# Performance work log

Hardware: AMD Instinct MI355X
Metric: run time of the kernel (lower is better)

Reference implementation:

```python
import jax, jax.numpy as jnp
import numpy as np

B, T, H = 2, 1024, 4096
HK, HV, DK, DV = 8, 32, 64, 64
VPK = HV // HK            # value heads per key head = 4
KEY_DIM = HK * DK         # 512
VAL_DIM = HV * DV         # 2048
CONV_DIM = 2 * KEY_DIM + VAL_DIM  # 3072
KSZ = 4
EPS = 1e-5
L2_EPS = 1e-6


def _l2norm(x):
    return x * jax.lax.rsqrt(jnp.sum(x * x, axis=-1, keepdims=True) + L2_EPS)


def setup_inputs() -> dict:
    key = jax.random.key(0)
    ks = jax.random.split(key, 8)
    s = 0.02
    return {
        "hidden_states": jax.random.normal(ks[0], (B, T, H), jnp.float32),
        "W_qkvz": jax.random.normal(ks[1], (H, 2 * KEY_DIM + 2 * VAL_DIM), jnp.float32) * s,
        "W_ba": jax.random.normal(ks[2], (H, 2 * HV), jnp.float32) * s,
        "conv_w": jax.random.normal(ks[3], (CONV_DIM, KSZ), jnp.float32) * 0.1,
        "dt_bias": jnp.ones((HV,), jnp.float32),
        "A_log": jnp.log(jax.random.uniform(ks[4], (HV,), jnp.float32, 1.0, 16.0)),
        "norm_w": jnp.ones((DV,), jnp.float32),
        "W_out": jax.random.normal(ks[5], (VAL_DIM, H), jnp.float32) * s,
    }


def _forward(hidden_states, W_qkvz, W_ba, conv_w, dt_bias, A_log, norm_w, W_out):
    # --- projections ---
    qkvz = hidden_states @ W_qkvz                       # [B,T,5120]
    ba = hidden_states @ W_ba                           # [B,T,64]
    # fix_query_key_value_ordering: per key head [q(Dk), k(Dk), v(vpk*Dv), z(vpk*Dv)]
    qkvz = qkvz.reshape(B, T, HK, 2 * DK + 2 * VPK * DV)
    q = qkvz[..., :DK]                                  # [B,T,HK,DK]
    k = qkvz[..., DK:2 * DK]
    v = qkvz[..., 2 * DK:2 * DK + VPK * DV].reshape(B, T, HV, DV)
    z = qkvz[..., 2 * DK + VPK * DV:].reshape(B, T, HV, DV)
    ba = ba.reshape(B, T, HK, 2 * VPK)
    b = ba[..., :VPK].reshape(B, T, HV)
    a = ba[..., VPK:].reshape(B, T, HV)

    # --- causal depthwise conv over concatenated qkv, then silu ---
    mixed = jnp.concatenate(
        [q.reshape(B, T, KEY_DIM), k.reshape(B, T, KEY_DIM), v.reshape(B, T, VAL_DIM)], axis=-1)
    padded = jnp.pad(mixed, ((0, 0), (KSZ - 1, 0), (0, 0)))
    conv = sum(padded[:, j:j + T, :] * conv_w[:, j] for j in range(KSZ))
    conv = jax.nn.silu(conv)
    q = conv[..., :KEY_DIM].reshape(B, T, HK, DK)
    k = conv[..., KEY_DIM:2 * KEY_DIM].reshape(B, T, HK, DK)
    v = conv[..., 2 * KEY_DIM:].reshape(B, T, HV, DV)

    # --- fused GDN gating: g = -exp(A_log)*softplus(a+dt_bias), beta = sigmoid(b) ---
    g = -jnp.exp(A_log) * jax.nn.softplus(a + dt_bias)  # [B,T,HV]
    beta = jax.nn.sigmoid(b)                            # [B,T,HV]

    # --- q/k l2 norm + scale, broadcast key heads to value heads ---
    q = _l2norm(q) * (DK ** -0.5)
    k = _l2norm(k)
    q = jnp.repeat(q, VPK, axis=2)                      # [B,T,HV,DK]
    k = jnp.repeat(k, VPK, axis=2)

    # --- gated delta-rule recurrence over time ---
    def step(S, inp):
        qt, kt, vt, gt, bt = inp                        # qt/kt [B,HV,DK], vt [B,HV,DV]
        S = S * jnp.exp(gt)[..., None, None]            # decay
        pred = jnp.einsum('bhk,bhkv->bhv', kt, S)
        delta = (vt - pred) * bt[..., None]
        S = S + jnp.einsum('bhk,bhv->bhkv', kt, delta)
        o = jnp.einsum('bhk,bhkv->bhv', qt, S)
        return S, o

    xs = (q.transpose(1, 0, 2, 3), k.transpose(1, 0, 2, 3), v.transpose(1, 0, 2, 3),
          g.transpose(1, 0, 2), beta.transpose(1, 0, 2))
    S0 = jnp.zeros((B, HV, DK, DV), q.dtype)
    _, o = jax.lax.scan(step, S0, xs)                   # [T,B,HV,DV]
    o = o.transpose(1, 0, 2, 3)                         # [B,T,HV,DV]

    # --- gated RMSNorm (norm before gate) + out projection ---
    o_n = o * jax.lax.rsqrt(jnp.mean(o * o, axis=-1, keepdims=True) + EPS) * norm_w
    o_n = o_n * jax.nn.silu(z)
    return o_n.reshape(B, T, VAL_DIM) @ W_out           # [B,T,H]


def reference(hidden_states, W_qkvz, W_ba, conv_w, dt_bias, A_log, norm_w, W_out):
    return _forward(hidden_states, W_qkvz, W_ba, conv_w, dt_bias, A_log, norm_w, W_out)
```

## Files before the change

### kernel.cpp

```cpp
#include <hip/hip_runtime.h>
#include <hip/hip_bf16.h>
#include <cstdint>
#include <cstddef>


typedef __attribute__((ext_vector_type(8))) short short8;
typedef __attribute__((ext_vector_type(4))) float f32x4;

__device__ __forceinline__ short f2bf(float f) {
  union { float f; unsigned u; } x; x.f = f;
  unsigned r = x.u + 0x7fffu + ((x.u >> 16) & 1u);
  return (short)(r >> 16);
}

__device__ __forceinline__ void gl_lds16(const short* g, short* l) {
  __builtin_amdgcn_global_load_lds(
      (const __attribute__((address_space(1))) void*)g,
      (__attribute__((address_space(3))) void*)l, 16, 0, 0);
}

__global__ __launch_bounds__(256) void to_bf16_kernel(const float* __restrict__ x,
                                                      short* __restrict__ y) {
  int i = blockIdx.x * 256 + threadIdx.x;
  float4 v = ((const float4*)x)[i];
  ushort4 r;
  r.x = (unsigned short)f2bf(v.x);
  r.y = (unsigned short)f2bf(v.y);
  r.z = (unsigned short)f2bf(v.z);
  r.w = (unsigned short)f2bf(v.w);
  ((ushort4*)y)[i] = r;
}

__global__ __launch_bounds__(256) void transpose_w1(const float* __restrict__ Wq,
                                                    const float* __restrict__ Wba,
                                                    short* __restrict__ Wt) {
  __shared__ float tile[32][33];
  int n0 = blockIdx.x * 32;
  int k0 = blockIdx.y * 32;
  int t = threadIdx.x;
  int r = t >> 5;
  int c = t & 31;
#pragma unroll
  for (int i = 0; i < 4; ++i) {
    int kl = r + i * 8;
    int n = n0 + c;
    float v = 0.f;
    if (n < 5120) v = Wq[(size_t)(k0 + kl) * 5120 + n];
    else if (n < 5184) v = Wba[(size_t)(k0 + kl) * 64 + (n - 5120)];
    tile[kl][c] = v;
  }
  __syncthreads();
#pragma unroll
  for (int i = 0; i < 4; ++i) {
    int nl = r + i * 8;
    int kl = c;
    Wt[(size_t)(n0 + nl) * 4096 + k0 + kl] = f2bf(tile[kl][nl]);
  }
}

__global__ __launch_bounds__(256) void transpose_w2(const float* __restrict__ W,
                                                    short* __restrict__ Wt) {
  __shared__ float tile[32][33];
  int n0 = blockIdx.x * 32;
  int k0 = blockIdx.y * 32;
  int t = threadIdx.x;
  int r = t >> 5;
  int c = t & 31;
#pragma unroll
  for (int i = 0; i < 4; ++i) {
    int kl = r + i * 8;
    tile[kl][c] = W[(size_t)(k0 + kl) * 4096 + n0 + c];
  }
  __syncthreads();
#pragma unroll
  for (int i = 0; i < 4; ++i) {
    int nl = r + i * 8;
    int kl = c;
    Wt[(size_t)(n0 + nl) * 2048 + k0 + kl] = f2bf(tile[kl][nl]);
  }
}

template <bool GUARD_N>
__global__ __launch_bounds__(256) void gemm128p(const short* __restrict__ A,
                                                const short* __restrict__ Bt,
                                                float* __restrict__ C,
                                                int N, int K, int MT) {
  __shared__ __align__(16) short As[3 * 4096];
  __shared__ __align__(16) short Bs[3 * 4096];
  const int tid = threadIdx.x;
  const int w = tid >> 6, lane = tid & 63;
  const int wm = w >> 1, wn = w & 1;

  const int nwg = gridDim.x;
  const int bid = blockIdx.x;
  const int swz = (bid & 7) * (nwg >> 3) + (bid >> 3);
  const int m0 = (swz % MT) * 128;
  const int n0 = (swz / MT) * 128;

  const int p0 = w * 64 + lane;
  const int rp0 = p0 >> 3, q0 = p0 & 7;
  const int mm0 = q0 ^ (rp0 & 7);
  const int srow = rp0 * 2 + (mm0 >> 2);
  const int scol = (mm0 & 3) << 3;
  const short* Ag = A + (size_t)(m0 + srow) * K + scol;
  const short* Bg = Bt + (size_t)(n0 + srow) * K + scol;
  const size_t rstep = (size_t)64 * K;

  const int fr = lane & 15;
  const int s = lane >> 4;
  int aoff[4], boff[4];
#pragma unroll
  for (int i = 0; i < 4; ++i) {
    int row = wm * 64 + i * 16 + fr;
    int rp = row >> 1;
    int q = (((row & 1) << 2) | s) ^ (rp & 7);
    aoff[i] = (rp * 8 + q) * 8;
  }
#pragma unroll
  for (int j = 0; j < 4; ++j) {
    int row = wn * 64 + j * 16 + fr;
    int rp = row >> 1;
    int q = (((row & 1) << 2) | s) ^ (rp & 7);
    boff[j] = (rp * 8 + q) * 8;
  }

  f32x4 acc[4][4];
#pragma unroll
  for (int i = 0; i < 4; ++i)
#pragma unroll
    for (int j = 0; j < 4; ++j) acc[i][j] = (f32x4){0.f, 0.f, 0.f, 0.f};

  const int NKT = K >> 5;

#define STAGE_A(kt, bb)                                                \
  { const short* g = Ag + (size_t)(kt) * 32;                           \
    gl_lds16(g,         &As[(bb) * 4096 + w * 512]);                   \
    gl_lds16(g + rstep, &As[(bb) * 4096 + 2048 + w * 512]); }
#define STAGE_B(kt, bb)                                                \
  { const short* g = Bg + (size_t)(kt) * 32;                           \
    gl_lds16(g,         &Bs[(bb) * 4096 + w * 512]);                   \
    gl_lds16(g + rstep, &Bs[(bb) * 4096 + 2048 + w * 512]); }

  STAGE_A(0, 0); STAGE_B(0, 0);
  STAGE_A(1, 1); STAGE_B(1, 1);
  asm volatile("s_waitcnt vmcnt(4)" ::: "memory");
  __builtin_amdgcn_s_barrier();
  __builtin_amdgcn_sched_barrier(0);

  int bi = 0;
  for (int kt = 0; kt < NKT; ++kt) {
    int bi2 = bi - 1; if (bi2 < 0) bi2 = 2;
    const short* Ab = &As[bi * 4096];
    const short* Bb = &Bs[bi * 4096];
    short8 af[2], bf[4];
#pragma unroll
    for (int i = 0; i < 2; ++i) af[i] = *(const short8*)&Ab[aoff[i]];
#pragma unroll
    for (int j = 0; j < 4; ++j) bf[j] = *(const short8*)&Bb[boff[j]];
    if (kt + 2 < NKT) STAGE_A(kt + 2, bi2);
    __builtin_amdgcn_s_barrier();
    asm volatile("s_waitcnt lgkmcnt(0)" ::: "memory");
    __builtin_amdgcn_sched_barrier(0);
    __builtin_amdgcn_s_setprio(1);
#pragma unroll
    for (int i = 0; i < 2; ++i)
#pragma unroll
      for (int j = 0; j < 4; ++j)
        acc[i][j] = __builtin_amdgcn_mfma_f32_16x16x32_bf16(af[i], bf[j], acc[i][j], 0, 0, 0);
    __builtin_amdgcn_s_setprio(0);
    __builtin_amdgcn_sched_barrier(0);
#pragma unroll
    for (int i = 0; i < 2; ++i) af[i] = *(const short8*)&Ab[aoff[i + 2]];
    if (kt + 2 < NKT) STAGE_B(kt + 2, bi2);
    if (kt < NKT - 2) { asm volatile("s_waitcnt vmcnt(4)" ::: "memory"); }
    else              { asm volatile("s_waitcnt vmcnt(0)" ::: "memory"); }
    __builtin_amdgcn_s_barrier();
    asm volatile("s_waitcnt lgkmcnt(0)" ::: "memory");
    __builtin_amdgcn_sched_barrier(0);
    __builtin_amdgcn_s_setprio(1);
#pragma unroll
    for (int i = 0; i < 2; ++i)
#pragma unroll
      for (int j = 0; j < 4; ++j)
        acc[i + 2][j] = __builtin_amdgcn_mfma_f32_16x16x32_bf16(af[i], bf[j], acc[i + 2][j], 0, 0, 0);
    __builtin_amdgcn_s_setprio(0);
    __builtin_amdgcn_sched_barrier(0);
    __builtin_amdgcn_s_barrier();
    ++bi; if (bi == 3) bi = 0;
  }
#undef STAGE_A
#undef STAGE_B

  const int rbase = (lane >> 4) << 2;
#pragma unroll
  for (int i = 0; i < 4; ++i) {
#pragma unroll
    for (int j = 0; j < 4; ++j) {
      int col = n0 + wn * 64 + j * 16 + fr;
      if (GUARD_N && col >= N) continue;
      int row = m0 + wm * 64 + i * 16 + rbase;
#pragma unroll
      for (int r = 0; r < 4; ++r)
        C[(size_t)(row + r) * N + col] = acc[i][j][r];
    }
  }
}

__global__ __launch_bounds__(256) void conv_kernel(const float* __restrict__ qkvz,
                                                   const float* __restrict__ conv_w,
                                                   float* __restrict__ mix) {
  __shared__ float sq[1024];
  __shared__ float scale[16];
  int bt = blockIdx.x;
  int t = bt & 1023;
  int tid = threadIdx.x;
  for (int c = tid; c < 3072; c += 256) {
    int col;
    if (c < 512) {
      col = (c >> 6) * 640 + (c & 63);
    } else if (c < 1024) {
      int c2 = c - 512;
      col = (c2 >> 6) * 640 + 64 + (c2 & 63);
    } else {
      int c3 = c - 1024;
      int hv = c3 >> 6;
      col = (hv >> 2) * 640 + 128 + (hv & 3) * 64 + (c3 & 63);
    }
    float acc = 0.f;
#pragma unroll
    for (int j = 0; j < 4; ++j) {
      int tt = t - 3 + j;
      if (tt >= 0) acc += qkvz[(size_t)(bt - 3 + j) * 5184 + col] * conv_w[c * 4 + j];
    }
    float sv = acc / (1.f + __expf(-acc));
    if (c < 1024)
      sq[c] = sv;
    else
      mix[(size_t)bt * 3072 + c] = sv;
  }
  __syncthreads();
  int g = tid >> 4, l = tid & 15;
  float p = 0.f;
#pragma unroll
  for (int i = 0; i < 4; ++i) {
    float v = sq[g * 64 + l * 4 + i];
    p += v * v;
  }
  p += __shfl_xor(p, 1);
  p += __shfl_xor(p, 2);
  p += __shfl_xor(p, 4);
  p += __shfl_xor(p, 8);
  if (l == 0) scale[g] = rsqrtf(p + 1e-6f);
  __syncthreads();
  for (int c = tid; c < 1024; c += 256) {
    float s = scale[c >> 6] * ((c < 512) ? 0.125f : 1.f);
    mix[(size_t)bt * 3072 + c] = sq[c] * s;
  }
}

__global__ __launch_bounds__(256) void gate_kernel(const float* __restrict__ qkvz,
                                                   const float* __restrict__ dt_bias,
                                                   const float* __restrict__ A_log,
                                                   float* __restrict__ gb,
                                                   float* __restrict__ beta) {
  int i = blockIdx.x * 256 + threadIdx.x;
  int hv = i & 31;
  int bt = i >> 5;
  int hk = hv >> 2, vp = hv & 3;
  const float* row = qkvz + (size_t)bt * 5184 + 5120 + hk * 8;
  float bv = row[vp];
  float av = row[4 + vp];
  float x = av + dt_bias[hv];
  float sp = (x > 20.f) ? x : log1pf(expf(x));
  gb[i] = -expf(A_log[hv]) * sp;
  beta[i] = 1.f / (1.f + expf(-bv));
}

__global__ __launch_bounds__(256) void precompute_kernel(
    const float* __restrict__ mix, const float* __restrict__ gbuf,
    const float* __restrict__ betab, float* __restrict__ Wbuf,
    float* __restrict__ Pbuf, float* __restrict__ Rbuf, float* __restrict__ cbuf) {
  __shared__ float Kt[64][68];
  __shared__ float Vb[64][68];
  __shared__ float AM[64][68];
  __shared__ float Mm[64][68];
  __shared__ float Tb[16][17];
  __shared__ float cs[64], bb[64];

  const int u = blockIdx.x;
  const int chunk = u & 15, hv = (u >> 4) & 31, b = u >> 9;
  const int hk = hv >> 2;
  const int t0g = b * 1024 + chunk * 64;
  const int tid = threadIdx.x;
  const int tr = tid >> 2, q4 = tid & 3;

  {
    const float* mrow = mix + (size_t)(t0g + tr) * 3072;
#pragma unroll
    for (int e = 0; e < 4; ++e) {
      int c0 = q4 * 16 + e * 4;
      float4 kv = *(const float4*)(mrow + 512 + hk * 64 + c0);
      Kt[c0 + 0][tr] = kv.x; Kt[c0 + 1][tr] = kv.y;
      Kt[c0 + 2][tr] = kv.z; Kt[c0 + 3][tr] = kv.w;
      *(float4*)&Vb[tr][c0] = *(const float4*)(mrow + 1024 + hv * 64 + c0);
    }
  }
  if (tid < 64) {
    cs[tid] = gbuf[(size_t)(t0g + tid) * 32 + hv];
    bb[tid] = betab[(size_t)(t0g + tid) * 32 + hv];
  }
  __syncthreads();
  for (int off = 1; off < 64; off <<= 1) {
    float v = 0.f;
    if (tid < 64 && tid >= off) v = cs[tid - off];
    __syncthreads();
    if (tid < 64) cs[tid] += v;
    __syncthreads();
  }
  if (tid < 64) cbuf[(size_t)u * 64 + tid] = cs[tid];

  {
    float acc[16];
#pragma unroll
    for (int i = 0; i < 16; ++i) acc[i] = 0.f;
    for (int d = 0; d < 64; ++d) {
      float kv = Kt[d][tr];
#pragma unroll
      for (int e = 0; e < 4; ++e) {
        float4 ks = *(const float4*)&Kt[d][q4 * 16 + e * 4];
        acc[e * 4 + 0] += kv * ks.x; acc[e * 4 + 1] += kv * ks.y;
        acc[e * 4 + 2] += kv * ks.z; acc[e * 4 + 3] += kv * ks.w;
      }
    }
    float bt_ = bb[tr], ct_ = cs[tr];
#pragma unroll
    for (int j = 0; j < 16; ++j) {
      int s = q4 * 16 + j;
      AM[tr][s] = (s < tr) ? bt_ * acc[j] * __expf(ct_ - cs[s]) : 0.f;
    }
  }
  __syncthreads();

  for (int i = tid; i < 64 * 68; i += 256) (&Mm[0][0])[i] = 0.f;
  __syncthreads();
  if (tid < 64) {
    int blk = tid >> 4, j = tid & 15, base = blk * 16;
    Mm[base][base + j] = (j == 0) ? 1.f : 0.f;
    for (int r = 1; r < 16; ++r) {
      float sum = 0.f;
      for (int s = 0; s < r; ++s) sum += AM[base + r][base + s] * Mm[base + s][base + j];
      Mm[base + r][base + j] = ((r == j) ? 1.f : 0.f) - sum;
    }
  }
  __syncthreads();
  for (int d = 1; d < 4; ++d) {
    for (int j = 0; j + d < 4; ++j) {
      int i = j + d;
      int r = tid >> 4, c = tid & 15;
      float tsum = 0.f;
      for (int kb = j; kb < i; ++kb)
        for (int uu = 0; uu < 16; ++uu)
          tsum += AM[i * 16 + r][kb * 16 + uu] * Mm[kb * 16 + uu][j * 16 + c];
      Tb[r][c] = tsum;
      __syncthreads();
      float msum = 0.f;
      for (int uu = 0; uu < 16; ++uu)
        msum += Mm[i * 16 + r][i * 16 + uu] * Tb[uu][c];
      __syncthreads();
      Mm[i * 16 + r][j * 16 + c] = -msum;
      __syncthreads();
    }
  }

  {
    const float* mrow = mix + (size_t)(t0g + tr) * 3072 + hk * 64;
#pragma unroll
    for (int e = 0; e < 4; ++e) {
      int c0 = q4 * 16 + e * 4;
      float4 qv = *(const float4*)(mrow + c0);
      AM[c0 + 0][tr] = qv.x; AM[c0 + 1][tr] = qv.y;
      AM[c0 + 2][tr] = qv.z; AM[c0 + 3][tr] = qv.w;
    }
  }
  __syncthreads();

  {
    float acc[16];
#pragma unroll
    for (int i = 0; i < 16; ++i) acc[i] = 0.f;
    for (int d = 0; d < 64; ++d) {
      float qv = AM[d][tr];
#pragma unroll
      for (int e = 0; e < 4; ++e) {
        float4 ks = *(const float4*)&Kt[d][q4 * 16 + e * 4];
        acc[e * 4 + 0] += qv * ks.x; acc[e * 4 + 1] += qv * ks.y;
        acc[e * 4 + 2] += qv * ks.z; acc[e * 4 + 3] += qv * ks.w;
      }
    }
    float ct_ = cs[tr];
#pragma unroll
    for (int e = 0; e < 4; ++e) {
      int s0 = q4 * 16 + e * 4;
      float4 pv;
      pv.x = (s0 + 0 <= tr) ? acc[e * 4 + 0] * __expf(ct_ - cs[s0 + 0]) : 0.f;
      pv.y = (s0 + 1 <= tr) ? acc[e * 4 + 1] * __expf(ct_ - cs[s0 + 1]) : 0.f;
      pv.z = (s0 + 2 <= tr) ? acc[e * 4 + 2] * __expf(ct_ - cs[s0 + 2]) : 0.f;
      pv.w = (s0 + 3 <= tr) ? acc[e * 4 + 3] * __expf(ct_ - cs[s0 + 3]) : 0.f;
      *(float4*)&Pbuf[(size_t)u * 4096 + tr * 64 + s0] = pv;
    }
  }
  __syncthreads();

  {
    float vals[16];
#pragma unroll
    for (int j = 0; j < 16; ++j) vals[j] = Kt[q4 * 16 + j][tr];
    float sc = bb[tr] * __expf(cs[tr]);
    __syncthreads();
#pragma unroll
    for (int j = 0; j < 16; ++j) Kt[tr][q4 * 16 + j] = vals[j] * sc;
  }
  __syncthreads();

  {
    float acc[16];
#pragma unroll
    for (int i = 0; i < 16; ++i) acc[i] = 0.f;
    for (int s = 0; s < 64; ++s) {
      float m = Mm[tr][s];
#pragma unroll
      for (int e = 0; e < 4; ++e) {
        float4 kk = *(const float4*)&Kt[s][q4 * 16 + e * 4];
        acc[e * 4 + 0] += m * kk.x; acc[e * 4 + 1] += m * kk.y;
        acc[e * 4 + 2] += m * kk.z; acc[e * 4 + 3] += m * kk.w;
      }
    }
#pragma unroll
    for (int e = 0; e < 4; ++e) {
      float4 wv = {acc[e * 4 + 0], acc[e * 4 + 1], acc[e * 4 + 2], acc[e * 4 + 3]};
      *(float4*)&Wbuf[(size_t)u * 4096 + tr * 64 + q4 * 16 + e * 4] = wv;
    }
  }
  {
    float acc[16];
#pragma unroll
    for (int i = 0; i < 16; ++i) acc[i] = 0.f;
    for (int s = 0; s < 64; ++s) {
      float m = Mm[tr][s] * bb[s];
#pragma unroll
      for (int e = 0; e < 4; ++e) {
        float4 vv = *(const float4*)&Vb[s][q4 * 16 + e * 4];
        acc[e * 4 + 0] += m * vv.x; acc[e * 4 + 1] += m * vv.y;
        acc[e * 4 + 2] += m * vv.z; acc[e * 4 + 3] += m * vv.w;
      }
    }
#pragma unroll
    for (int e = 0; e < 4; ++e) {
      float4 rv = {acc[e * 4 + 0], acc[e * 4 + 1], acc[e * 4 + 2], acc[e * 4 + 3]};
      *(float4*)&Rbuf[(size_t)u * 4096 + tr * 64 + q4 * 16 + e * 4] = rv;
    }
  }
}

__global__ __launch_bounds__(256) void precompute2_kernel(
    const float* __restrict__ mix, const float* __restrict__ cbuf,
    float* __restrict__ Wbuf, float* __restrict__ Pbuf, float* __restrict__ Rbuf,
    float* __restrict__ Hbuf) {
  __shared__ float At[64][132];
  __shared__ float Bsm[64][188];

  const int u = blockIdx.x;
  const int chunk = u & 15, hv = (u >> 4) & 31, b = u >> 9;
  const int hk = hv >> 2;
  const int t0g = b * 1024 + chunk * 64;
  const int tid = threadIdx.x;
  const int tr = tid >> 2, q4 = tid & 3;

  const float c63 = cbuf[(size_t)u * 64 + 63];
  const float csr = cbuf[(size_t)u * 64 + tr];
  const float sKv = __expf(c63 - csr);

  {
    const float* Pr = Pbuf + (size_t)u * 4096 + tr * 64;
#pragma unroll
    for (int e = 0; e < 4; ++e) {
      int k0 = q4 * 16 + e * 4;
      float4 p4 = *(const float4*)(Pr + k0);
      At[k0 + 0][tr] = p4.x; At[k0 + 1][tr] = p4.y;
      At[k0 + 2][tr] = p4.z; At[k0 + 3][tr] = p4.w;
    }
    const float* Kr = mix + (size_t)(t0g + tr) * 3072 + 512 + hk * 64;
#pragma unroll
    for (int e = 0; e < 4; ++e) {
      int n = q4 * 16 + e * 4;
      float4 k4 = *(const float4*)(Kr + n);
      float4 o4 = {k4.x * sKv, k4.y * sKv, k4.z * sKv, k4.w * sKv};
      *(float4*)&At[tr][64 + n] = o4;
    }
  }
  {
    const float* Wr = Wbuf + (size_t)u * 4096 + tr * 64;
    const float* Rr = Rbuf + (size_t)u * 4096 + tr * 64;
#pragma unroll
    for (int e = 0; e < 4; ++e) {
      int n = q4 * 16 + e * 4;
      int cp = n + ((n >> 3) << 2);
      *(float4*)&Bsm[tr][cp] = *(const float4*)(Wr + n);
      *(float4*)&Bsm[tr][cp + 96] = *(const float4*)(Rr + n);
    }
  }
  __syncthreads();

  const int m0 = (tid >> 4) << 3;
  const int n0 = (tid & 15) << 3;
  const int cb = n0 + ((n0 >> 3) << 2);
  float acc[8][8];
#pragma unroll
  for (int i = 0; i < 8; ++i)
#pragma unroll
    for (int j = 0; j < 8; ++j) acc[i][j] = 0.f;

  for (int k = 0; k < 64; ++k) {
    float4 a0 = *(const float4*)&At[k][m0];
    float4 a1 = *(const float4*)&At[k][m0 + 4];
    float4 b0 = *(const float4*)&Bsm[k][cb];
    float4 b1 = *(const float4*)&Bsm[k][cb + 4];
    float am[8] = {a0.x, a0.y, a0.z, a0.w, a1.x, a1.y, a1.z, a1.w};
    float bn[8] = {b0.x, b0.y, b0.z, b0.w, b1.x, b1.y, b1.z, b1.w};
#pragma unroll
    for (int i = 0; i < 8; ++i)
#pragma unroll
      for (int j = 0; j < 8; ++j) acc[i][j] += am[i] * bn[j];
  }

  if (m0 < 64) {
    if (n0 < 64) {
#pragma unroll
      for (int i = 0; i < 8; ++i) {
        int t = m0 + i;
        float ee = __expf(cbuf[(size_t)u * 64 + t]);
        const float* Qr = mix + (size_t)(t0g + t) * 3072 + hk * 64 + n0;
        float4 q0 = *(const float4*)(Qr);
        float4 q1 = *(const float4*)(Qr + 4);
        float4 g0 = {q0.x * ee - acc[i][0], q0.y * ee - acc[i][1],
                     q0.z * ee - acc[i][2], q0.w * ee - acc[i][3]};
        float4 g1 = {q1.x * ee - acc[i][4], q1.y * ee - acc[i][5],
                     q1.z * ee - acc[i][6], q1.w * ee - acc[i][7]};
        float* dst = Wbuf + (size_t)u * 4096 + t * 64 + n0;
        *(float4*)dst = g0; *(float4*)(dst + 4) = g1;
      }
    } else {
#pragma unroll
      for (int i = 0; i < 8; ++i) {
        float* dst = Rbuf + (size_t)u * 4096 + (m0 + i) * 64 + (n0 - 64);
        float4 r0 = {acc[i][0], acc[i][1], acc[i][2], acc[i][3]};
        float4 r1 = {acc[i][4], acc[i][5], acc[i][6], acc[i][7]};
        *(float4*)dst = r0; *(float4*)(dst + 4) = r1;
      }
    }
  } else {
    if (n0 < 64) {
#pragma unroll
      for (int i = 0; i < 8; ++i) {
        float* dst = Hbuf + (size_t)u * 4096 + (m0 - 64 + i) * 64 + n0;
        float4 h0 = {acc[i][0], acc[i][1], acc[i][2], acc[i][3]};
        float4 h1 = {acc[i][4], acc[i][5], acc[i][6], acc[i][7]};
        *(float4*)dst = h0; *(float4*)(dst + 4) = h1;
      }
    } else {
#pragma unroll
      for (int i = 0; i < 8; ++i) {
        float* dst = Pbuf + (size_t)u * 4096 + (m0 - 64 + i) * 64 + (n0 - 64);
        float4 k0v = {acc[i][0], acc[i][1], acc[i][2], acc[i][3]};
        float4 k1v = {acc[i][4], acc[i][5], acc[i][6], acc[i][7]};
        *(float4*)dst = k0v; *(float4*)(dst + 4) = k1v;
      }
    }
  }
}

__global__ __launch_bounds__(1024) void chunk_scan_kernel(
    const float* __restrict__ Gbuf, const float* __restrict__ Hbuf,
    const float* __restrict__ ORbuf, const float* __restrict__ KRbuf,
    const float* __restrict__ cbuf, float* __restrict__ o) {
  __shared__ float Gs[64][72], Hs[64][72];
  __shared__ float St[16][68];

  const int bid = blockIdx.x;
  const int vs = bid & 3, hv = (bid >> 2) & 31, b = bid >> 7;
  const int bh = b * 32 + hv;
  const int ubase = bh * 16;
  const int tid = threadIdx.x;
  const int tr = tid >> 4, cc = tid & 15;

  (&St[0][0])[tid] = 0.f;
  if (tid < 64) (&St[0][0])[1024 + tid] = 0.f;

  float4 GN, HN;
  float ORn = 0.f, KRn = 0.f, e63n = 0.f;

#define ISSUE(ch)                                                               \
  {                                                                             \
    size_t uu = (size_t)(ubase + (ch));                                         \
    GN = ((const float4*)(Gbuf + uu * 4096))[tid];                              \
    HN = ((const float4*)(Hbuf + uu * 4096))[tid];                              \
    ORn = ORbuf[uu * 4096 + tr * 64 + vs * 16 + cc];                            \
    KRn = KRbuf[uu * 4096 + tr * 64 + vs * 16 + cc];                            \
    e63n = cbuf[uu * 64 + 63];                                                  \
  }

  ISSUE(0);
  *(float4*)&Gs[tr][cc * 4] = GN;
  *(float4*)&Hs[tr][cc * 4] = HN;
  float ORv = ORn, KRv = KRn;
  float e63 = __expf(e63n);
  __syncthreads();

  for (int c = 0; c < 16; ++c) {
    if (c < 15) ISSUE(c + 1);
    float op = ORv, sn = KRv;
    float sold = St[cc][tr];
#pragma unroll
    for (int i = 0; i < 16; ++i) {
      float4 g4 = *(const float4*)&Gs[tr][i * 4];
      float4 h4 = *(const float4*)&Hs[tr][i * 4];
      float4 s4 = *(const float4*)&St[cc][i * 4];
      op += g4.x * s4.x + g4.y * s4.y + g4.z * s4.z + g4.w * s4.w;
      sn -= h4.x * s4.x + h4.y * s4.y + h4.z * s4.z + h4.w * s4.w;
    }
    o[((size_t)(bh * 4 + vs) * 1024 + c * 64 + tr) * 16 + cc] = op;
    float snew = sold * e63 + sn;
    __syncthreads();
    St[cc][tr] = snew;
    if (c < 15) {
      *(float4*)&Gs[tr][cc * 4] = GN;
      *(float4*)&Hs[tr][cc * 4] = HN;
      ORv = ORn; KRv = KRn; e63 = __expf(e63n);
    }
    __syncthreads();
  }
#undef ISSUE
}

__global__ __launch_bounds__(256) void rms_gate_kernel(const float* __restrict__ o,
                                                       const float* __restrict__ qkvz,
                                                       const float* __restrict__ norm_w,
                                                       short* __restrict__ on) {
  int bid = blockIdx.x;
  int bh = bid >> 8;
  int tg = bid & 255;
  int b = bh >> 5, hv = bh & 31;
  int t = tg * 4 + (threadIdx.x >> 6);
  int d = threadIdx.x & 63;
  int bt = b * 1024 + t;
  int hk = hv >> 2, vp = hv & 3;
  float x = o[((size_t)(bh * 4 + (d >> 4)) * 1024 + t) * 16 + (d & 15)];
  float ss = x * x;
  ss += __shfl_xor(ss, 1);
  ss += __shfl_xor(ss, 2);
  ss += __shfl_xor(ss, 4);
  ss += __shfl_xor(ss, 8);
  ss += __shfl_xor(ss, 16);
  ss += __shfl_xor(ss, 32);
  float sc = rsqrtf(ss * (1.f / 64.f) + 1e-5f);
  float z = qkvz[(size_t)bt * 5184 + hk * 640 + 384 + vp * 64 + d];
  float val = x * sc * norm_w[d] * (z / (1.f + __expf(-z)));
  on[((size_t)bt * 32 + hv) * 64 + d] = f2bf(val);
}

extern "C" void kernel_launch(void* const* d_in, const int* in_sizes, int n_in,
                              void* d_out, int out_size, void* d_ws, size_t ws_size,
                              hipStream_t stream) {
  const float* hidden = (const float*)d_in[0];
  const float* W_qkvz = (const float*)d_in[1];
  const float* W_ba = (const float*)d_in[2];
  const float* conv_w = (const float*)d_in[3];
  const float* dt_bias = (const float*)d_in[4];
  const float* A_log = (const float*)d_in[5];
  const float* norm_w = (const float*)d_in[6];
  const float* W_out = (const float*)d_in[7];
  float* out = (float*)d_out;

  char* ws = (char*)d_ws;
  short* A_bf = (short*)(ws + 0);
  float* Hbuf = (float*)(ws + 0);
  short* Wt1 = (short*)(ws + 16777216);
  short* Wt2 = (short*)(ws + 59768832);
  float* qkvz = (float*)(ws + 76546048);
  float* mix = (float*)(ws + 119013376);
  float* gbuf = (float*)(ws + 144179200);
  float* beta = (float*)(ws + 144441344);
  float* o = (float*)(ws + 144703488);
  short* on = (short*)(ws + 161480704);
  float* Wbuf = (float*)(ws + 169869312);
  float* Pbuf = (float*)(ws + 186646528);
  float* Rbuf = (float*)(ws + 203423744);
  float* cbuf = (float*)(ws + 220200960);

  to_bf16_kernel<<<8192, 256, 0, stream>>>(hidden, A_bf);
  transpose_w1<<<dim3(164, 128), 256, 0, stream>>>(W_qkvz, W_ba, Wt1);
  transpose_w2<<<dim3(128, 64), 256, 0, stream>>>(W_out, Wt2);
  gemm128p<true><<<656, 256, 0, stream>>>(A_bf, Wt1, qkvz, 5184, 4096, 16);
  conv_kernel<<<2048, 256, 0, stream>>>(qkvz, conv_w, mix);
  gate_kernel<<<256, 256, 0, stream>>>(qkvz, dt_bias, A_log, gbuf, beta);
  precompute_kernel<<<1024, 256, 0, stream>>>(mix, gbuf, beta, Wbuf, Pbuf, Rbuf, cbuf);
  precompute2_kernel<<<1024, 256, 0, stream>>>(mix, cbuf, Wbuf, Pbuf, Rbuf, Hbuf);
  chunk_scan_kernel<<<256, 1024, 0, stream>>>(Wbuf, Hbuf, Rbuf, Pbuf, cbuf, o);
  rms_gate_kernel<<<16384, 256, 0, stream>>>(o, qkvz, norm_w, on);
  gemm128p<false><<<512, 256, 0, stream>>>(on, Wt2, out, 4096, 2048, 16);
}
```

Baseline: 529.6 us.

## Use 256x128 tile GEMM for the input projection

Adds a new bf16 MFMA GEMM kernel with 256x128 output tiles (each wave computing 128x64) and a triple-buffered LDS pipeline. The A-fragment loads are split into two halves interleaved with the B staging, and the QKVZ projection is switched to it with half as many workgroups. The larger tile is meant to cut global/LDS traffic per FLOP and raise arithmetic intensity. In exchange it uses more registers and LDS per block, and with 328 blocks the GPU may be less evenly occupied.

```diff
diff --git a/kernel.cpp b/kernel.cpp
--- a/kernel.cpp
+++ b/kernel.cpp
@@ -77,6 +77,134 @@
     int nl = r + i * 8;
     int kl = c;
     Wt[(size_t)(n0 + nl) * 2048 + k0 + kl] = f2bf(tile[kl][nl]);
+  }
+}
+
+template <bool GUARD_N>
+__global__ __launch_bounds__(256) void gemm256x128p(const short* __restrict__ A,
+                                                    const short* __restrict__ Bt,
+                                                    float* __restrict__ C,
+                                                    int N, int K, int MT) {
+  __shared__ __align__(16) short As[3 * 8192];
+  __shared__ __align__(16) short Bs[3 * 4096];
+  const int tid = threadIdx.x;
+  const int w = tid >> 6, lane = tid & 63;
+  const int wm = w >> 1, wn = w & 1;
+
+  const int nwg = gridDim.x;
+  const int bid = blockIdx.x;
+  const int swz = (bid & 7) * (nwg >> 3) + (bid >> 3);
+  const int m0 = (swz % MT) * 256;
+  const int n0 = (swz / MT) * 128;
+
+  const int p0 = w * 64 + lane;
+  const int rp0 = p0 >> 3, q0 = p0 & 7;
+  const int mm0 = q0 ^ (rp0 & 7);
+  const int srow = rp0 * 2 + (mm0 >> 2);
+  const int scol = (mm0 & 3) << 3;
+  const short* Ag = A + (size_t)(m0 + srow) * K + scol;
+  const short* Bg = Bt + (size_t)(n0 + srow) * K + scol;
+  const size_t rstep = (size_t)64 * K;
+
+  const int fr = lane & 15;
+  const int s = lane >> 4;
+  int aoff[8], boff[4];
+#pragma unroll
+  for (int i = 0; i < 8; ++i) {
+    int row = wm * 128 + i * 16 + fr;
+    int rp = row >> 1;
+    int q = (((row & 1) << 2) | s) ^ (rp & 7);
+    aoff[i] = (rp * 8 + q) * 8;
+  }
+#pragma unroll
+  for (int j = 0; j < 4; ++j) {
+    int row = wn * 64 + j * 16 + fr;
+    int rp = row >> 1;
+    int q = (((row & 1) << 2) | s) ^ (rp & 7);
+    boff[j] = (rp * 8 + q) * 8;
+  }
+
+  f32x4 acc[8][4];
+#pragma unroll
+  for (int i = 0; i < 8; ++i)
+#pragma unroll
+    for (int j = 0; j < 4; ++j) acc[i][j] = (f32x4){0.f, 0.f, 0.f, 0.f};
+
+  const int NKT = K >> 5;
+
+#define STAGE_A(kt, bb)                                                \
+  { const short* g = Ag + (size_t)(kt) * 32;                           \
+    gl_lds16(g,             &As[(bb) * 8192 + w * 512]);               \
+    gl_lds16(g + rstep,     &As[(bb) * 8192 + 2048 + w * 512]);        \
+    gl_lds16(g + 2 * rstep, &As[(bb) * 8192 + 4096 + w * 512]);        \
+    gl_lds16(g + 3 * rstep, &As[(bb) * 8192 + 6144 + w * 512]); }
+#define STAGE_B(kt, bb)                                                \
+  { const short* g = Bg + (size_t)(kt) * 32;                           \
+    gl_lds16(g,         &Bs[(bb) * 4096 + w * 512]);                   \
+    gl_lds16(g + rstep, &Bs[(bb) * 4096 + 2048 + w * 512]); }
+
+  STAGE_A(0, 0); STAGE_B(0, 0);
+  STAGE_A(1, 1); STAGE_B(1, 1);
+  asm volatile("s_waitcnt vmcnt(6)" ::: "memory");
+  __builtin_amdgcn_s_barrier();
+  __builtin_amdgcn_sched_barrier(0);
+
+  int bi = 0;
+  for (int kt = 0; kt < NKT; ++kt) {
+    int bi2 = bi - 1; if (bi2 < 0) bi2 = 2;
+    const short* Ab = &As[bi * 8192];
+    const short* Bb = &Bs[bi * 4096];
+    short8 af[4], bf[4];
+#pragma unroll
+    for (int i = 0; i < 4; ++i) af[i] = *(const short8*)&Ab[aoff[i]];
+#pragma unroll
+    for (int j = 0; j < 4; ++j) bf[j] = *(const short8*)&Bb[boff[j]];
+    if (kt + 2 < NKT) STAGE_A(kt + 2, bi2);
+    __builtin_amdgcn_s_barrier();
+    asm volatile("s_waitcnt lgkmcnt(0)" ::: "memory");
+    __builtin_amdgcn_sched_barrier(0);
+    __builtin_amdgcn_s_setprio(1);
+#pragma unroll
+    for (int i = 0; i < 4; ++i)
+#pragma unroll
+      for (int j = 0; j < 4; ++j)
+        acc[i][j] = __builtin_amdgcn_mfma_f32_16x16x32_bf16(af[i], bf[j], acc[i][j], 0, 0, 0);
+    __builtin_amdgcn_s_setprio(0);
+    __builtin_amdgcn_sched_barrier(0);
+#pragma unroll
+    for (int i = 0; i < 4; ++i) af[i] = *(const short8*)&Ab[aoff[i + 4]];
+    if (kt + 2 < NKT) STAGE_B(kt + 2, bi2);
+    if (kt < NKT - 2) { asm volatile("s_waitcnt vmcnt(6)" ::: "memory"); }
+    else              { asm volatile("s_waitcnt vmcnt(0)" ::: "memory"); }
+    __builtin_amdgcn_s_barrier();
+    asm volatile("s_waitcnt lgkmcnt(0)" ::: "memory");
+    __builtin_amdgcn_sched_barrier(0);
+    __builtin_amdgcn_s_setprio(1);
+#pragma unroll
+    for (int i = 0; i < 4; ++i)
+#pragma unroll
+      for (int j = 0; j < 4; ++j)
+        acc[i + 4][j] = __builtin_amdgcn_mfma_f32_16x16x32_bf16(af[i], bf[j], acc[i + 4][j], 0, 0, 0);
+    __builtin_amdgcn_s_setprio(0);
+    __builtin_amdgcn_sched_barrier(0);
+    __builtin_amdgcn_s_barrier();
+    ++bi; if (bi == 3) bi = 0;
+  }
+#undef STAGE_A
+#undef STAGE_B
+
+  const int rbase = (lane >> 4) << 2;
+#pragma unroll
+  for (int i = 0; i < 8; ++i) {
+#pragma unroll
+    for (int j = 0; j < 4; ++j) {
+      int col = n0 + wn * 64 + j * 16 + fr;
+      if (GUARD_N && col >= N) continue;
+      int row = m0 + wm * 128 + i * 16 + rbase;
+#pragma unroll
+      for (int r = 0; r < 4; ++r)
+        C[(size_t)(row + r) * N + col] = acc[i][j][r];
+    }
   }
 }
 
@@ -700,7 +828,7 @@
   to_bf16_kernel<<<8192, 256, 0, stream>>>(hidden, A_bf);
   transpose_w1<<<dim3(164, 128), 256, 0, stream>>>(W_qkvz, W_ba, Wt1);
   transpose_w2<<<dim3(128, 64), 256, 0, stream>>>(W_out, Wt2);
-  gemm128p<true><<<656, 256, 0, stream>>>(A_bf, Wt1, qkvz, 5184, 4096, 16);
+  gemm256x128p<true><<<328, 256, 0, stream>>>(A_bf, Wt1, qkvz, 5184, 4096, 8);
   conv_kernel<<<2048, 256, 0, stream>>>(qkvz, conv_w, mix);
   gate_kernel<<<256, 256, 0, stream>>>(qkvz, dt_bias, A_log, gbuf, beta);
   precompute_kernel<<<1024, 256, 0, stream>>>(mix, gbuf, beta, Wbuf, Pbuf, Rbuf, cbuf);
```

Measured after the change: 534.8 us. About the same (+1.0%).

## Use two-wave 128x128 GEMM tiles and halve chunk-scan threads with two columns each

Applied to the files above, without the earlier changes.

The GEMM drops from 4 waves to 2 waves per 128x128 tile. Each wave now computes a 64x128 sub-tile with a 4x8 MFMA accumulator grid, loads 4 A and 8 B fragments per k-step, and issues 4 global-to-LDS loads per stage. The chunk scan kernel goes from 1024 to 512 threads, each computing two state columns, so every G/H fragment read from LDS is reused twice, and the Gs/Hs padding changes. The aim is more work per wave and less LDS traffic per flop, at the cost of higher register pressure (128 accumulator floats per lane) and fewer waves to hide latency.

```diff
diff --git a/kernel.cpp b/kernel.cpp
--- a/kernel.cpp
+++ b/kernel.cpp
@@ -81,15 +81,14 @@
 }
 
 template <bool GUARD_N>
-__global__ __launch_bounds__(256) void gemm128p(const short* __restrict__ A,
-                                                const short* __restrict__ Bt,
-                                                float* __restrict__ C,
-                                                int N, int K, int MT) {
+__global__ __launch_bounds__(128) void gemm128w2(const short* __restrict__ A,
+                                                 const short* __restrict__ Bt,
+                                                 float* __restrict__ C,
+                                                 int N, int K, int MT) {
   __shared__ __align__(16) short As[3 * 4096];
   __shared__ __align__(16) short Bs[3 * 4096];
   const int tid = threadIdx.x;
   const int w = tid >> 6, lane = tid & 63;
-  const int wm = w >> 1, wn = w & 1;
 
   const int nwg = gridDim.x;
   const int bid = blockIdx.x;
@@ -97,53 +96,56 @@
   const int m0 = (swz % MT) * 128;
   const int n0 = (swz / MT) * 128;
 
-  const int p0 = w * 64 + lane;
-  const int rp0 = p0 >> 3, q0 = p0 & 7;
+  const int rp0 = tid >> 3, q0 = tid & 7;
   const int mm0 = q0 ^ (rp0 & 7);
   const int srow = rp0 * 2 + (mm0 >> 2);
   const int scol = (mm0 & 3) << 3;
   const short* Ag = A + (size_t)(m0 + srow) * K + scol;
   const short* Bg = Bt + (size_t)(n0 + srow) * K + scol;
-  const size_t rstep = (size_t)64 * K;
+  const size_t rstep = (size_t)32 * K;
 
   const int fr = lane & 15;
   const int s = lane >> 4;
-  int aoff[4], boff[4];
+  int aoff[4], boff[8];
 #pragma unroll
   for (int i = 0; i < 4; ++i) {
-    int row = wm * 64 + i * 16 + fr;
+    int row = w * 64 + i * 16 + fr;
     int rp = row >> 1;
     int q = (((row & 1) << 2) | s) ^ (rp & 7);
     aoff[i] = (rp * 8 + q) * 8;
   }
 #pragma unroll
-  for (int j = 0; j < 4; ++j) {
-    int row = wn * 64 + j * 16 + fr;
+  for (int j = 0; j < 8; ++j) {
+    int row = j * 16 + fr;
     int rp = row >> 1;
     int q = (((row & 1) << 2) | s) ^ (rp & 7);
     boff[j] = (rp * 8 + q) * 8;
   }
 
-  f32x4 acc[4][4];
+  f32x4 acc[4][8];
 #pragma unroll
   for (int i = 0; i < 4; ++i)
 #pragma unroll
-    for (int j = 0; j < 4; ++j) acc[i][j] = (f32x4){0.f, 0.f, 0.f, 0.f};
+    for (int j = 0; j < 8; ++j) acc[i][j] = (f32x4){0.f, 0.f, 0.f, 0.f};
 
   const int NKT = K >> 5;
 
-#define STAGE_A(kt, bb)                                                \
-  { const short* g = Ag + (size_t)(kt) * 32;                           \
-    gl_lds16(g,         &As[(bb) * 4096 + w * 512]);                   \
-    gl_lds16(g + rstep, &As[(bb) * 4096 + 2048 + w * 512]); }
-#define STAGE_B(kt, bb)                                                \
-  { const short* g = Bg + (size_t)(kt) * 32;                           \
-    gl_lds16(g,         &Bs[(bb) * 4096 + w * 512]);                   \
-    gl_lds16(g + rstep, &Bs[(bb) * 4096 + 2048 + w * 512]); }
+#define STAGE_A(kt, bb)                                                  \
+  { const short* g = Ag + (size_t)(kt) * 32;                             \
+    gl_lds16(g,             &As[(bb) * 4096 + (w << 9)]);                \
+    gl_lds16(g + rstep,     &As[(bb) * 4096 + 1024 + (w << 9)]);         \
+    gl_lds16(g + 2 * rstep, &As[(bb) * 4096 + 2048 + (w << 9)]);         \
+    gl_lds16(g + 3 * rstep, &As[(bb) * 4096 + 3072 + (w << 9)]); }
+#define STAGE_B(kt, bb)                                                  \
+  { const short* g = Bg + (size_t)(kt) * 32;                             \
+    gl_lds16(g,             &Bs[(bb) * 4096 + (w << 9)]);                \
+    gl_lds16(g + rstep,     &Bs[(bb) * 4096 + 1024 + (w << 9)]);         \
+    gl_lds16(g + 2 * rstep, &Bs[(bb) * 4096 + 2048 + (w << 9)]);         \
+    gl_lds16(g + 3 * rstep, &Bs[(bb) * 4096 + 3072 + (w << 9)]); }
 
   STAGE_A(0, 0); STAGE_B(0, 0);
   STAGE_A(1, 1); STAGE_B(1, 1);
-  asm volatile("s_waitcnt vmcnt(4)" ::: "memory");
+  asm volatile("s_waitcnt vmcnt(8)" ::: "memory");
   __builtin_amdgcn_s_barrier();
   __builtin_amdgcn_sched_barrier(0);
 
@@ -152,9 +154,9 @@
     int bi2 = bi - 1; if (bi2 < 0) bi2 = 2;
     const short* Ab = &As[bi * 4096];
     const short* Bb = &Bs[bi * 4096];
-    short8 af[2], bf[4];
-#pragma unroll
-    for (int i = 0; i < 2; ++i) af[i] = *(const short8*)&Ab[aoff[i]];
+    short8 af[4], bf[4];
+#pragma unroll
+    for (int i = 0; i < 4; ++i) af[i] = *(const short8*)&Ab[aoff[i]];
 #pragma unroll
     for (int j = 0; j < 4; ++j) bf[j] = *(const short8*)&Bb[boff[j]];
     if (kt + 2 < NKT) STAGE_A(kt + 2, bi2);
@@ -163,26 +165,26 @@
     __builtin_amdgcn_sched_barrier(0);
     __builtin_amdgcn_s_setprio(1);
 #pragma unroll
-    for (int i = 0; i < 2; ++i)
+    for (int i = 0; i < 4; ++i)
 #pragma unroll
       for (int j = 0; j < 4; ++j)
         acc[i][j] = __builtin_amdgcn_mfma_f32_16x16x32_bf16(af[i], bf[j], acc[i][j], 0, 0, 0);
     __builtin_amdgcn_s_setprio(0);
     __builtin_amdgcn_sched_barrier(0);
 #pragma unroll
-    for (int i = 0; i < 2; ++i) af[i] = *(const short8*)&Ab[aoff[i + 2]];
+    for (int j = 0; j < 4; ++j) bf[j] = *(const short8*)&Bb[boff[j + 4]];
     if (kt + 2 < NKT) STAGE_B(kt + 2, bi2);
-    if (kt < NKT - 2) { asm volatile("s_waitcnt vmcnt(4)" ::: "memory"); }
+    if (kt < NKT - 2) { asm volatile("s_waitcnt vmcnt(8)" ::: "memory"); }
     else              { asm volatile("s_waitcnt vmcnt(0)" ::: "memory"); }
     __builtin_amdgcn_s_barrier();
     asm volatile("s_waitcnt lgkmcnt(0)" ::: "memory");
     __builtin_amdgcn_sched_barrier(0);
     __builtin_amdgcn_s_setprio(1);
 #pragma unroll
-    for (int i = 0; i < 2; ++i)
+    for (int i = 0; i < 4; ++i)
 #pragma unroll
       for (int j = 0; j < 4; ++j)
-        acc[i + 2][j] = __builtin_amdgcn_mfma_f32_16x16x32_bf16(af[i], bf[j], acc[i + 2][j], 0, 0, 0);
+        acc[i][j + 4] = __builtin_amdgcn_mfma_f32_16x16x32_bf16(af[i], bf[j], acc[i][j + 4], 0, 0, 0);
     __builtin_amdgcn_s_setprio(0);
     __builtin_amdgcn_sched_barrier(0);
     __builtin_amdgcn_s_barrier();
@@ -195,10 +197,10 @@
 #pragma unroll
   for (int i = 0; i < 4; ++i) {
 #pragma unroll
-    for (int j = 0; j < 4; ++j) {
-      int col = n0 + wn * 64 + j * 16 + fr;
+    for (int j = 0; j < 8; ++j) {
+      int col = n0 + j * 16 + fr;
       if (GUARD_N && col >= N) continue;
-      int row = m0 + wm * 64 + i * 16 + rbase;
+      int row = m0 + w * 64 + i * 16 + rbase;
 #pragma unroll
       for (int r = 0; r < 4; ++r)
         C[(size_t)(row + r) * N + col] = acc[i][j][r];
@@ -579,11 +581,11 @@
   }
 }
 
-__global__ __launch_bounds__(1024) void chunk_scan_kernel(
+__global__ __launch_bounds__(512) void chunk_scan_kernel(
     const float* __restrict__ Gbuf, const float* __restrict__ Hbuf,
     const float* __restrict__ ORbuf, const float* __restrict__ KRbuf,
     const float* __restrict__ cbuf, float* __restrict__ o) {
-  __shared__ float Gs[64][72], Hs[64][72];
+  __shared__ float Gs[64][68], Hs[64][68];
   __shared__ float St[16][68];
 
   const int bid = blockIdx.x;
@@ -591,55 +593,73 @@
   const int bh = b * 32 + hv;
   const int ubase = bh * 16;
   const int tid = threadIdx.x;
-  const int tr = tid >> 4, cc = tid & 15;
-
-  (&St[0][0])[tid] = 0.f;
-  if (tid < 64) (&St[0][0])[1024 + tid] = 0.f;
-
-  float4 GN, HN;
-  float ORn = 0.f, KRn = 0.f, e63n = 0.f;
+  const int tr = tid >> 3, q8 = tid & 7;
+  const int c0 = q8 * 2, c1 = q8 * 2 + 1;
+
+  for (int i = tid; i < 16 * 68; i += 512) (&St[0][0])[i] = 0.f;
+
+  float4 GN[2], HN[2];
+  float2 ORn, KRn;
+  float e63n = 0.f;
 
 #define ISSUE(ch)                                                               \
   {                                                                             \
     size_t uu = (size_t)(ubase + (ch));                                         \
-    GN = ((const float4*)(Gbuf + uu * 4096))[tid];                              \
-    HN = ((const float4*)(Hbuf + uu * 4096))[tid];                              \
-    ORn = ORbuf[uu * 4096 + tr * 64 + vs * 16 + cc];                            \
-    KRn = KRbuf[uu * 4096 + tr * 64 + vs * 16 + cc];                            \
+    _Pragma("unroll") for (int i = 0; i < 2; ++i) {                             \
+      GN[i] = ((const float4*)(Gbuf + uu * 4096))[tid + 512 * i];               \
+      HN[i] = ((const float4*)(Hbuf + uu * 4096))[tid + 512 * i];               \
+    }                                                                           \
+    ORn = *(const float2*)(ORbuf + uu * 4096 + tr * 64 + vs * 16 + q8 * 2);     \
+    KRn = *(const float2*)(KRbuf + uu * 4096 + tr * 64 + vs * 16 + q8 * 2);     \
     e63n = cbuf[uu * 64 + 63];                                                  \
   }
 
+#define COMMIT()                                                                \
+  {                                                                             \
+    _Pragma("unroll") for (int i = 0; i < 2; ++i) {                             \
+      int flat = (tid + 512 * i) * 4;                                           \
+      int rr = flat >> 6, cc = flat & 63;                                       \
+      *(float4*)&Gs[rr][cc] = GN[i];                                            \
+      *(float4*)&Hs[rr][cc] = HN[i];                                            \
+    }                                                                           \
+  }
+
   ISSUE(0);
-  *(float4*)&Gs[tr][cc * 4] = GN;
-  *(float4*)&Hs[tr][cc * 4] = HN;
-  float ORv = ORn, KRv = KRn;
+  COMMIT();
+  float2 ORv = ORn, KRv = KRn;
   float e63 = __expf(e63n);
   __syncthreads();
 
   for (int c = 0; c < 16; ++c) {
     if (c < 15) ISSUE(c + 1);
-    float op = ORv, sn = KRv;
-    float sold = St[cc][tr];
+    float op0 = ORv.x, op1 = ORv.y, sn0 = KRv.x, sn1 = KRv.y;
+    float sold0 = St[c0][tr], sold1 = St[c1][tr];
 #pragma unroll
     for (int i = 0; i < 16; ++i) {
       float4 g4 = *(const float4*)&Gs[tr][i * 4];
       float4 h4 = *(const float4*)&Hs[tr][i * 4];
-      float4 s4 = *(const float4*)&St[cc][i * 4];
-      op += g4.x * s4.x + g4.y * s4.y + g4.z * s4.z + g4.w * s4.w;
-      sn -= h4.x * s4.x + h4.y * s4.y + h4.z * s4.z + h4.w * s4.w;
-    }
-    o[((size_t)(bh * 4 + vs) * 1024 + c * 64 + tr) * 16 + cc] = op;
-    float snew = sold * e63 + sn;
+      float4 sa = *(const float4*)&St[c0][i * 4];
+      float4 sb = *(const float4*)&St[c1][i * 4];
+      op0 += g4.x * sa.x + g4.y * sa.y + g4.z * sa.z + g4.w * sa.w;
+      op1 += g4.x * sb.x + g4.y * sb.y + g4.z * sb.z + g4.w * sb.w;
+      sn0 -= h4.x * sa.x + h4.y * sa.y + h4.z * sa.z + h4.w * sa.w;
+      sn1 -= h4.x * sb.x + h4.y * sb.y + h4.z * sb.z + h4.w * sb.w;
+    }
+    *(float2*)&o[((size_t)(bh * 4 + vs) * 1024 + c * 64 + tr) * 16 + q8 * 2] =
+        (float2){op0, op1};
+    float snew0 = sold0 * e63 + sn0;
+    float snew1 = sold1 * e63 + sn1;
     __syncthreads();
-    St[cc][tr] = snew;
+    St[c0][tr] = snew0;
+    St[c1][tr] = snew1;
     if (c < 15) {
-      *(float4*)&Gs[tr][cc * 4] = GN;
-      *(float4*)&Hs[tr][cc * 4] = HN;
+      COMMIT();
       ORv = ORn; KRv = KRn; e63 = __expf(e63n);
     }
     __syncthreads();
   }
 #undef ISSUE
+#undef COMMIT
 }
 
 __global__ __launch_bounds__(256) void rms_gate_kernel(const float* __restrict__ o,
@@ -700,12 +720,12 @@
   to_bf16_kernel<<<8192, 256, 0, stream>>>(hidden, A_bf);
   transpose_w1<<<dim3(164, 128), 256, 0, stream>>>(W_qkvz, W_ba, Wt1);
   transpose_w2<<<dim3(128, 64), 256, 0, stream>>>(W_out, Wt2);
-  gemm128p<true><<<656, 256, 0, stream>>>(A_bf, Wt1, qkvz, 5184, 4096, 16);
+  gemm128w2<true><<<656, 128, 0, stream>>>(A_bf, Wt1, qkvz, 5184, 4096, 16);
   conv_kernel<<<2048, 256, 0, stream>>>(qkvz, conv_w, mix);
   gate_kernel<<<256, 256, 0, stream>>>(qkvz, dt_bias, A_log, gbuf, beta);
   precompute_kernel<<<1024, 256, 0, stream>>>(mix, gbuf, beta, Wbuf, Pbuf, Rbuf, cbuf);
   precompute2_kernel<<<1024, 256, 0, stream>>>(mix, cbuf, Wbuf, Pbuf, Rbuf, Hbuf);
-  chunk_scan_kernel<<<256, 1024, 0, stream>>>(Wbuf, Hbuf, Rbuf, Pbuf, cbuf, o);
+  chunk_scan_kernel<<<256, 512, 0, stream>>>(Wbuf, Hbuf, Rbuf, Pbuf, cbuf, o);
   rms_gate_kernel<<<16384, 256, 0, stream>>>(o, qkvz, norm_w, on);
-  gemm128p<false><<<512, 256, 0, stream>>>(on, Wt2, out, 4096, 2048, 16);
-}
+  gemm128w2<false><<<512, 128, 0, stream>>>(on, Wt2, out, 4096, 2048, 16);
+}
```

Measured after the change: 556.9 us. 5.1% more time.
